# Kernel optimization log

Measured on AMD Instinct MI355X. Metric: run time of the kernel, lower is better.

The kernel has to match this reference:

```python
import jax, jax.numpy as jnp
import numpy as np

N, E, F_IN, H, G, C = 200000, 1000000, 64, 64, 512, 10
EPS = 1e-5


def setup_inputs() -> dict:
    key = jax.random.key(0)
    ks = jax.random.split(key, 16)
    x = jax.random.normal(ks[0], (N, F_IN), dtype=jnp.float32)
    edge_index = jax.random.randint(ks[1], (2, E), 0, N, dtype=jnp.int32)
    batch = jnp.sort(jax.random.randint(ks[2], (N,), 0, G, dtype=jnp.int32))
    def glorot(k, shape):
        lim = np.sqrt(6.0 / (shape[0] + shape[1]))
        return jax.random.uniform(k, shape, jnp.float32, -lim, lim)
    return {
        "x": x, "edge_index": edge_index, "batch": batch,
        "W1": glorot(ks[3], (F_IN, H)), "b1": jnp.zeros((H,), jnp.float32),
        "g1": jnp.ones((H,), jnp.float32), "be1": jnp.zeros((H,), jnp.float32),
        "W2": glorot(ks[4], (H, H)), "b2": jnp.zeros((H,), jnp.float32),
        "g2": jnp.ones((H,), jnp.float32), "be2": jnp.zeros((H,), jnp.float32),
        "lw1": glorot(ks[5], (H, H // 2)), "lb1": jnp.zeros((H // 2,), jnp.float32),
        "lw2": glorot(ks[6], (H // 2, C)), "lb2": jnp.zeros((C,), jnp.float32),
    }


def _gcn_conv(h, src, dst, norm, W, b):
    # PyG GCNConv: linear transform, then normalized gather-scatter aggregation
    h = h @ W                                   # [N, H]
    msg = h[src] * norm[:, None]                # [E+N, H] gather + scale
    out = jax.ops.segment_sum(msg, dst, num_segments=N)  # scatter-add
    return out + b


def _bn_relu(h, g, be):
    m = h.mean(axis=0)
    v = jnp.var(h, axis=0)                      # biased var, as torch BN training
    return jax.nn.relu((h - m) * jax.lax.rsqrt(v + EPS) * g + be)


def reference(x, edge_index, batch, W1, b1, g1, be1, W2, b2, g2, be2,
              lw1, lb1, lw2, lb2):
    loop = jnp.arange(N, dtype=edge_index.dtype)
    src = jnp.concatenate([edge_index[0], loop])  # add self-loops
    dst = jnp.concatenate([edge_index[1], loop])
    deg = jax.ops.segment_sum(jnp.ones_like(src, jnp.float32), dst, num_segments=N)
    dinv = jax.lax.rsqrt(jnp.maximum(deg, 1.0))
    norm = dinv[src] * dinv[dst]                  # sym normalization

    h = _bn_relu(_gcn_conv(x, src, dst, norm, W1, b1), g1, be1)
    prev = h
    h = _bn_relu(_gcn_conv(h, src, dst, norm, W2, b2), g2, be2)
    h = h + prev                                  # residual (dims match)

    # global mean pool over graphs
    sums = jax.ops.segment_sum(h, batch, num_segments=G)        # [G, H]
    cnt = jax.ops.segment_sum(jnp.ones((N,), jnp.float32), batch, num_segments=G)
    pooled = sums / jnp.maximum(cnt, 1.0)[:, None]

    z = jax.nn.relu(pooled @ lw1 + lb1)
    logits = z @ lw2 + lb2                        # [G, C]
    return jax.nn.log_softmax(logits, axis=-1)
```

## Files before the change

kernel.cpp:

```cpp
#include <hip/hip_runtime.h>
#include <hip/hip_bf16.h>
#include <cstdint>
#include <cstddef>

typedef unsigned short u16;
typedef unsigned int u32;
typedef __attribute__((ext_vector_type(8))) short bf16x8;
typedef __attribute__((ext_vector_type(4))) float f32x4;

__device__ __forceinline__ float bf2f(u16 u) {
    return __uint_as_float(((u32)u) << 16);
}
__device__ __forceinline__ float bflo(u32 u) { return __uint_as_float(u << 16); }
__device__ __forceinline__ float bfhi(u32 u) { return __uint_as_float(u & 0xFFFF0000u); }
__device__ __forceinline__ u32 f2bf(float f) {
    u32 b = __float_as_uint(f);
    return (b + 0x7FFFu + ((b >> 16) & 1u)) >> 16;
}

#define CAP 32


__global__ __launch_bounds__(256) void k_fused1(
        const float* __restrict__ X, const float* __restrict__ W,
        const int* __restrict__ ei, int E,
        int* __restrict__ cnt, int* __restrict__ bucket,
        u16* __restrict__ Yb, int nrows, int gemmBlocks) {
    if ((int)blockIdx.x >= gemmBlocks) {
        int e = (blockIdx.x - gemmBlocks) * 256 + threadIdx.x;
        if (e < E) {
            int s = ei[e], d = ei[E + e];
            int pos = atomicAdd(&cnt[d], 1);
            if (pos < CAP) bucket[(size_t)d * CAP + pos] = s;
        }
        return;
    }
    int lane = threadIdx.x & 63;
    int wave = threadIdx.x >> 6;
    int row0 = blockIdx.x * 64 + wave * 16;
    if (row0 >= nrows) return;
    int lrow = lane & 15;
    int lgrp = lane >> 4;

    bf16x8 bfrag[4][2];
#pragma unroll
    for (int c = 0; c < 4; ++c)
#pragma unroll
        for (int h = 0; h < 2; ++h) {
            bf16x8 t;
#pragma unroll
            for (int j = 0; j < 8; ++j)
                t[j] = (short)f2bf(W[(h * 32 + lgrp * 8 + j) * 64 + c * 16 + lrow]);
            bfrag[c][h] = t;
        }

    int arow = min(row0 + lrow, nrows - 1);
    const float* xr = X + (size_t)arow * 64 + lgrp * 8;
    bf16x8 afrag[2];
#pragma unroll
    for (int h = 0; h < 2; ++h) {
        bf16x8 t;
#pragma unroll
        for (int j = 0; j < 8; ++j) t[j] = (short)f2bf(xr[h * 32 + j]);
        afrag[h] = t;
    }

    f32x4 acc[4] = {};
#pragma unroll
    for (int h = 0; h < 2; ++h)
#pragma unroll
        for (int c = 0; c < 4; ++c)
            acc[c] = __builtin_amdgcn_mfma_f32_16x16x32_bf16(afrag[h], bfrag[c][h], acc[c], 0, 0, 0);

#pragma unroll
    for (int j = 0; j < 4; ++j) {
        int r = row0 + lgrp * 4 + j;
        if (r < nrows)
#pragma unroll
            for (int c = 0; c < 4; ++c)
                Yb[(size_t)r * 64 + c * 16 + lrow] = (u16)f2bf(acc[c][j]);
    }
}


__global__ void k_scalelb(u16* __restrict__ HAb, const int* __restrict__ cnt,
                          const int* __restrict__ batch, int* __restrict__ lbound,
                          int N, int G) {
    int idx = blockIdx.x * blockDim.x + threadIdx.x;
    int stride = gridDim.x * blockDim.x;
    int n16 = N * 16;
    uint2* p = (uint2*)HAb;
    for (int i = idx; i < n16; i += stride) {
        int r = i >> 4;
        float dv = rsqrtf((float)(cnt[r] + 1));
        uint2 v = p[i];
        uint2 o;
        o.x = f2bf(bflo(v.x) * dv) | (f2bf(bfhi(v.x) * dv) << 16);
        o.y = f2bf(bflo(v.y) * dv) | (f2bf(bfhi(v.y) * dv) << 16);
        p[i] = o;
    }
    for (int i = idx; i < N; i += stride) {
        int b  = batch[i];
        int bp = (i > 0) ? batch[i - 1] : -1;
        for (int g = bp + 1; g <= b; ++g) lbound[g] = i;
        if (i == N - 1) for (int g = b + 1; g <= G; ++g) lbound[g] = N;
    }
}


__global__ __launch_bounds__(256) void k_gemm2(
        const u16* __restrict__ Xb, const float* __restrict__ W,
        const float* __restrict__ st, const float* __restrict__ g,
        const float* __restrict__ be, const int* __restrict__ cnt,
        u16* __restrict__ Yb, int nrows) {
    __shared__ float ssc[128];
    if (threadIdx.x < 64) {
        int f = threadIdx.x;
        float invn = 1.f / (float)nrows;
        float m   = st[f] * invn;
        float var = st[64 + f] * invn - m * m;
        float scale = g[f] * rsqrtf(var + 1e-5f);
        ssc[f]      = scale;
        ssc[64 + f] = be[f] - m * scale;
    }
    __syncthreads();

    int lane = threadIdx.x & 63;
    int wave = threadIdx.x >> 6;
    int row0 = blockIdx.x * 64 + wave * 16;
    if (row0 >= nrows) return;
    int lrow = lane & 15;
    int lgrp = lane >> 4;

    bf16x8 bfrag[4][2];
#pragma unroll
    for (int c = 0; c < 4; ++c)
#pragma unroll
        for (int h = 0; h < 2; ++h) {
            bf16x8 t;
#pragma unroll
            for (int j = 0; j < 8; ++j)
                t[j] = (short)f2bf(W[(h * 32 + lgrp * 8 + j) * 64 + c * 16 + lrow]);
            bfrag[c][h] = t;
        }

    int arow = min(row0 + lrow, nrows - 1);
    const u16* xr = Xb + (size_t)arow * 64 + lgrp * 8;
    bf16x8 afrag[2];
#pragma unroll
    for (int h = 0; h < 2; ++h) {
        bf16x8 t;
#pragma unroll
        for (int j = 0; j < 8; ++j) {
            int k = h * 32 + lgrp * 8 + j;
            float v = bf2f(xr[h * 32 + j]);
            v = fmaxf(fmaf(v, ssc[k], ssc[64 + k]), 0.f);
            t[j] = (short)f2bf(v);
        }
        afrag[h] = t;
    }

    f32x4 acc[4] = {};
#pragma unroll
    for (int h = 0; h < 2; ++h)
#pragma unroll
        for (int c = 0; c < 4; ++c)
            acc[c] = __builtin_amdgcn_mfma_f32_16x16x32_bf16(afrag[h], bfrag[c][h], acc[c], 0, 0, 0);

#pragma unroll
    for (int j = 0; j < 4; ++j) {
        int r = row0 + lgrp * 4 + j;
        if (r < nrows) {
            float dv = rsqrtf((float)(cnt[r] + 1));
#pragma unroll
            for (int c = 0; c < 4; ++c)
                Yb[(size_t)r * 64 + c * 16 + lrow] = (u16)f2bf(acc[c][j] * dv);
        }
    }
}


__global__ __launch_bounds__(256) void k_gather(
        const u16* __restrict__ HA, const int* __restrict__ cnt,
        const int* __restrict__ bucket, u16* __restrict__ outb,
        float* __restrict__ st, int N) {
    int lane = threadIdx.x & 63;
    int wid  = (blockIdx.x * blockDim.x + threadIdx.x) >> 6;
    int nw   = (gridDim.x * blockDim.x) >> 6;
    float s_ = 0.f, sq_ = 0.f;
    int nb4 = (N + 3) >> 2;
    for (int bt = wid; bt < nb4; bt += nw) {
        int r0 = __builtin_amdgcn_readfirstlane(bt << 2);
        int r1 = min(r0 + 1, N - 1);
        int r2 = min(r0 + 2, N - 1);
        int r3 = min(r0 + 3, N - 1);
        int c0 = cnt[r0], c1 = cnt[r1], c2 = cnt[r2], c3 = cnt[r3];
        int n0 = min(c0, CAP), n1 = min(c1, CAP), n2 = min(c2, CAP), n3 = min(c3, CAP);
        float a0 = bf2f(HA[(size_t)r0 * 64 + lane]);
        float a1 = bf2f(HA[(size_t)r1 * 64 + lane]);
        float a2 = bf2f(HA[(size_t)r2 * 64 + lane]);
        float a3 = bf2f(HA[(size_t)r3 * 64 + lane]);
        const int* bp0 = bucket + (size_t)r0 * CAP;
        const int* bp1 = bucket + (size_t)r1 * CAP;
        const int* bp2 = bucket + (size_t)r2 * CAP;
        const int* bp3 = bucket + (size_t)r3 * CAP;
        int nmax = max(max(n0, n1), max(n2, n3));
        for (int c = 0; c < nmax; c += 8) {
#define IDS(I) \
            int e##I##0 = (c + 0 < n##I) ? bp##I[c + 0] : 0; \
            int e##I##1 = (c + 1 < n##I) ? bp##I[c + 1] : 0; \
            int e##I##2 = (c + 2 < n##I) ? bp##I[c + 2] : 0; \
            int e##I##3 = (c + 3 < n##I) ? bp##I[c + 3] : 0; \
            int e##I##4 = (c + 4 < n##I) ? bp##I[c + 4] : 0; \
            int e##I##5 = (c + 5 < n##I) ? bp##I[c + 5] : 0; \
            int e##I##6 = (c + 6 < n##I) ? bp##I[c + 6] : 0; \
            int e##I##7 = (c + 7 < n##I) ? bp##I[c + 7] : 0;
            IDS(0) IDS(1) IDS(2) IDS(3)
#undef IDS
#define LD(I) \
            float v##I##0 = bf2f(HA[(size_t)e##I##0 * 64 + lane]); \
            float v##I##1 = bf2f(HA[(size_t)e##I##1 * 64 + lane]); \
            float v##I##2 = bf2f(HA[(size_t)e##I##2 * 64 + lane]); \
            float v##I##3 = bf2f(HA[(size_t)e##I##3 * 64 + lane]); \
            float v##I##4 = bf2f(HA[(size_t)e##I##4 * 64 + lane]); \
            float v##I##5 = bf2f(HA[(size_t)e##I##5 * 64 + lane]); \
            float v##I##6 = bf2f(HA[(size_t)e##I##6 * 64 + lane]); \
            float v##I##7 = bf2f(HA[(size_t)e##I##7 * 64 + lane]);
            LD(0) LD(1) LD(2) LD(3)
#undef LD
#define ACCUM(I) \
            a##I += (c + 0 < n##I) ? v##I##0 : 0.f; \
            a##I += (c + 1 < n##I) ? v##I##1 : 0.f; \
            a##I += (c + 2 < n##I) ? v##I##2 : 0.f; \
            a##I += (c + 3 < n##I) ? v##I##3 : 0.f; \
            a##I += (c + 4 < n##I) ? v##I##4 : 0.f; \
            a##I += (c + 5 < n##I) ? v##I##5 : 0.f; \
            a##I += (c + 6 < n##I) ? v##I##6 : 0.f; \
            a##I += (c + 7 < n##I) ? v##I##7 : 0.f;
            ACCUM(0) ACCUM(1) ACCUM(2) ACCUM(3)
#undef ACCUM
        }
        float d0 = rsqrtf((float)(c0 + 1));
        float d1 = rsqrtf((float)(c1 + 1));
        float d2 = rsqrtf((float)(c2 + 1));
        float d3 = rsqrtf((float)(c3 + 1));
        {
            u16 u = (u16)f2bf(a0 * d0);
            outb[(size_t)r0 * 64 + lane] = u;
            float vr = bf2f(u); s_ += vr; sq_ += vr * vr;
        }
        if (r0 + 1 < N) {
            u16 u = (u16)f2bf(a1 * d1);
            outb[(size_t)r1 * 64 + lane] = u;
            float vr = bf2f(u); s_ += vr; sq_ += vr * vr;
        }
        if (r0 + 2 < N) {
            u16 u = (u16)f2bf(a2 * d2);
            outb[(size_t)r2 * 64 + lane] = u;
            float vr = bf2f(u); s_ += vr; sq_ += vr * vr;
        }
        if (r0 + 3 < N) {
            u16 u = (u16)f2bf(a3 * d3);
            outb[(size_t)r3 * 64 + lane] = u;
            float vr = bf2f(u); s_ += vr; sq_ += vr * vr;
        }
    }
    __shared__ float ls[4][64], lq[4][64];
    int grp = threadIdx.x >> 6;
    ls[grp][lane] = s_; lq[grp][lane] = sq_;
    __syncthreads();
    if (grp == 0) {
        s_  = ls[0][lane] + ls[1][lane] + ls[2][lane] + ls[3][lane];
        sq_ = lq[0][lane] + lq[1][lane] + lq[2][lane] + lq[3][lane];
        unsafeAtomicAdd(&st[lane], s_);
        unsafeAtomicAdd(&st[64 + lane], sq_);
    }
}


__global__ void k_pool(const u16* __restrict__ rb2, const float* __restrict__ st2,
                       const float* __restrict__ g2, const float* __restrict__ be2,
                       const u16* __restrict__ rb1, const float* __restrict__ st1,
                       const float* __restrict__ g1, const float* __restrict__ be1,
                       const int* __restrict__ batch, float* __restrict__ psum, int N) {
    __shared__ float s1[128], s2[128];
    if (threadIdx.x < 64) {
        int f = threadIdx.x;
        float invn = 1.f / (float)N;
        float m   = st2[f] * invn;
        float var = st2[64 + f] * invn - m * m;
        float scale = g2[f] * rsqrtf(var + 1e-5f);
        s2[f] = scale; s2[64 + f] = be2[f] - m * scale;
    } else if (threadIdx.x < 128) {
        int f = threadIdx.x - 64;
        float invn = 1.f / (float)N;
        float m   = st1[f] * invn;
        float var = st1[64 + f] * invn - m * m;
        float scale = g1[f] * rsqrtf(var + 1e-5f);
        s1[f] = scale; s1[64 + f] = be1[f] - m * scale;
    }
    __syncthreads();

    int lane = threadIdx.x & 63;
    int wv   = (blockIdx.x * blockDim.x + threadIdx.x) >> 6;
    int r0   = wv * 64;
    if (r0 >= N) return;
    int rend = min(r0 + 64, N);
    int bv = (r0 + lane < N) ? batch[r0 + lane] : -1;
    float s2a = s2[lane], s2b = s2[64 + lane];
    float s1a = s1[lane], s1b = s1[64 + lane];
    float acc = 0.f;
    int cur = __shfl(bv, 0, 64);
    for (int r = r0; r < rend; ++r) {
        int b = __shfl(bv, r - r0, 64);
        if (b != cur) {
            unsafeAtomicAdd(&psum[(size_t)cur * 64 + lane], acc);
            acc = 0.f; cur = b;
        }
        float v2 = fmaxf(fmaf(bf2f(rb2[(size_t)r * 64 + lane]), s2a, s2b), 0.f);
        float v1 = fmaxf(fmaf(bf2f(rb1[(size_t)r * 64 + lane]), s1a, s1b), 0.f);
        acc += v1 + v2;
    }
    unsafeAtomicAdd(&psum[(size_t)cur * 64 + lane], acc);
}


__global__ void k_head(const float* __restrict__ psum, const int* __restrict__ lbound,
                       const float* __restrict__ lw1, const float* __restrict__ lb1,
                       const float* __restrict__ lw2, const float* __restrict__ lb2,
                       float* __restrict__ out, int G) {
    int g = blockIdx.x * blockDim.x + threadIdx.x;
    if (g >= G) return;
    float cnt = (float)(lbound[g + 1] - lbound[g]);
    float inv = 1.f / fmaxf(cnt, 1.f);
    float p[64];
#pragma unroll
    for (int f = 0; f < 64; ++f) p[f] = psum[(size_t)g * 64 + f] * inv;
    float z[32];
#pragma unroll
    for (int j = 0; j < 32; ++j) {
        float a = lb1[j];
#pragma unroll
        for (int f = 0; f < 64; ++f) a = fmaf(p[f], lw1[f * 32 + j], a);
        z[j] = fmaxf(a, 0.f);
    }
    float lg[10];
    float mx = -1e30f;
#pragma unroll
    for (int c = 0; c < 10; ++c) {
        float a = lb2[c];
#pragma unroll
        for (int j = 0; j < 32; ++j) a = fmaf(z[j], lw2[j * 10 + c], a);
        lg[c] = a;
        mx = fmaxf(mx, a);
    }
    float se = 0.f;
#pragma unroll
    for (int c = 0; c < 10; ++c) se += expf(lg[c] - mx);
    float lse = logf(se) + mx;
#pragma unroll
    for (int c = 0; c < 10; ++c) out[(size_t)g * 10 + c] = lg[c] - lse;
}


extern "C" void kernel_launch(void* const* d_in, const int* in_sizes, int n_in,
                              void* d_out, int out_size, void* d_ws, size_t ws_size,
                              hipStream_t stream) {
    const float* x    = (const float*)d_in[0];
    const int*   ei   = (const int*)d_in[1];
    const int*   batch= (const int*)d_in[2];
    const float* W1   = (const float*)d_in[3];
    const float* g1   = (const float*)d_in[5];
    const float* be1  = (const float*)d_in[6];
    const float* W2   = (const float*)d_in[7];
    const float* g2   = (const float*)d_in[9];
    const float* be2  = (const float*)d_in[10];
    const float* lw1  = (const float*)d_in[11];
    const float* lb1  = (const float*)d_in[12];
    const float* lw2  = (const float*)d_in[13];
    const float* lb2  = (const float*)d_in[14];
    float* out = (float*)d_out;

    const int N = in_sizes[2];
    const int E = in_sizes[1] / 2;
    const int C = 10;
    const int G = out_size / C;

    char* wp = (char*)d_ws;
    auto carve = [&wp](size_t bytes) -> char* {
        uintptr_t u = ((uintptr_t)wp + 63) & ~(uintptr_t)63;
        char* r = (char*)u;
        wp = r + bytes;
        return r;
    };
    int*   cnt   = (int*)carve((size_t)N * 4);
    float* st1   = (float*)carve(128 * 4);
    float* st2   = (float*)carve(128 * 4);
    float* psum  = (float*)carve((size_t)G * 64 * 4);
    size_t zone  = (char*)(psum + (size_t)G * 64) - (char*)cnt;
    int*   lbound= (int*)carve((size_t)(G + 1) * 4);
    int*   bucket= (int*)carve((size_t)N * CAP * 4);
    u16*   HAbf  = (u16*)carve((size_t)N * 64 * 2);
    u16*   Rb1   = (u16*)carve((size_t)N * 64 * 2);
    u16*   Rb2   = (u16*)carve((size_t)N * 64 * 2);

    hipMemsetAsync(cnt, 0, zone, stream);

    const int gemmBlocks = (N + 63) / 64;
    const int fillBlocks = (E + 255) / 256;

    k_fused1<<<gemmBlocks + fillBlocks, 256, 0, stream>>>(
        x, W1, ei, E, cnt, bucket, HAbf, N, gemmBlocks);

    k_scalelb<<<2048, 256, 0, stream>>>(HAbf, cnt, batch, lbound, N, G);

    k_gather<<<4096, 256, 0, stream>>>(HAbf, cnt, bucket, Rb1, st1, N);

    k_gemm2<<<gemmBlocks, 256, 0, stream>>>(Rb1, W2, st1, g1, be1, cnt, HAbf, N);

    k_gather<<<4096, 256, 0, stream>>>(HAbf, cnt, bucket, Rb2, st2, N);

    {
        int waves = (N + 63) / 64;
        int blocks = (waves + 3) / 4;
        k_pool<<<blocks, 256, 0, stream>>>(Rb2, st2, g2, be2, Rb1, st1, g1, be1,
                                           batch, psum, N);
    }

    k_head<<<(G + 255) / 256, 256, 0, stream>>>(psum, lbound, lw1, lb1, lw2, lb2, out, G);
}
```

Baseline: 415.6 us.

## Transpose edge buckets to slot-major and fold degree scaling into first GEMM

Stores neighbor buckets slot-major so the gather loads four rows' neighbor ids with one vector read per slot. Splits the bucket fill from the first GEMM so the GEMM can apply the inverse-sqrt-degree scaling in its epilogue, removing the separate rescale pass over the feature matrix. Graph boundaries for mean pooling are now found by binary search in the head kernel instead of a precomputed array. Bucket fill writes become strided across nodes, and the extra kernel boundary serializes the fill and GEMM.

```diff
diff --git a/kernel.cpp b/kernel.cpp
--- a/kernel.cpp
+++ b/kernel.cpp
@@ -21,20 +21,19 @@
 #define CAP 32
 
 
-__global__ __launch_bounds__(256) void k_fused1(
+__global__ void k_bfill(const int* __restrict__ ei, int E, int N,
+                        int* __restrict__ cnt, int* __restrict__ bucket) {
+    int e = blockIdx.x * blockDim.x + threadIdx.x;
+    if (e >= E) return;
+    int s = ei[e], d = ei[E + e];
+    int pos = atomicAdd(&cnt[d], 1);
+    if (pos < CAP) bucket[(size_t)pos * N + d] = s;
+}
+
+
+__global__ __launch_bounds__(256) void k_gemm1(
         const float* __restrict__ X, const float* __restrict__ W,
-        const int* __restrict__ ei, int E,
-        int* __restrict__ cnt, int* __restrict__ bucket,
-        u16* __restrict__ Yb, int nrows, int gemmBlocks) {
-    if ((int)blockIdx.x >= gemmBlocks) {
-        int e = (blockIdx.x - gemmBlocks) * 256 + threadIdx.x;
-        if (e < E) {
-            int s = ei[e], d = ei[E + e];
-            int pos = atomicAdd(&cnt[d], 1);
-            if (pos < CAP) bucket[(size_t)d * CAP + pos] = s;
-        }
-        return;
-    }
+        const int* __restrict__ cnt, u16* __restrict__ Yb, int nrows) {
     int lane = threadIdx.x & 63;
     int wave = threadIdx.x >> 6;
     int row0 = blockIdx.x * 64 + wave * 16;
@@ -75,35 +74,12 @@
 #pragma unroll
     for (int j = 0; j < 4; ++j) {
         int r = row0 + lgrp * 4 + j;
-        if (r < nrows)
+        if (r < nrows) {
+            float dv = rsqrtf((float)(cnt[r] + 1));
 #pragma unroll
             for (int c = 0; c < 4; ++c)
-                Yb[(size_t)r * 64 + c * 16 + lrow] = (u16)f2bf(acc[c][j]);
-    }
-}
-
-
-__global__ void k_scalelb(u16* __restrict__ HAb, const int* __restrict__ cnt,
-                          const int* __restrict__ batch, int* __restrict__ lbound,
-                          int N, int G) {
-    int idx = blockIdx.x * blockDim.x + threadIdx.x;
-    int stride = gridDim.x * blockDim.x;
-    int n16 = N * 16;
-    uint2* p = (uint2*)HAb;
-    for (int i = idx; i < n16; i += stride) {
-        int r = i >> 4;
-        float dv = rsqrtf((float)(cnt[r] + 1));
-        uint2 v = p[i];
-        uint2 o;
-        o.x = f2bf(bflo(v.x) * dv) | (f2bf(bfhi(v.x) * dv) << 16);
-        o.y = f2bf(bflo(v.y) * dv) | (f2bf(bfhi(v.y) * dv) << 16);
-        p[i] = o;
-    }
-    for (int i = idx; i < N; i += stride) {
-        int b  = batch[i];
-        int bp = (i > 0) ? batch[i - 1] : -1;
-        for (int g = bp + 1; g <= b; ++g) lbound[g] = i;
-        if (i == N - 1) for (int g = b + 1; g <= G; ++g) lbound[g] = N;
+                Yb[(size_t)r * 64 + c * 16 + lrow] = (u16)f2bf(acc[c][j] * dv);
+        }
     }
 }
 
@@ -189,6 +165,7 @@
     int nw   = (gridDim.x * blockDim.x) >> 6;
     float s_ = 0.f, sq_ = 0.f;
     int nb4 = (N + 3) >> 2;
+    u32 nm1 = (u32)(N - 1);
     for (int bt = wid; bt < nb4; bt += nw) {
         int r0 = __builtin_amdgcn_readfirstlane(bt << 2);
         int r1 = min(r0 + 1, N - 1);
@@ -200,44 +177,33 @@
         float a1 = bf2f(HA[(size_t)r1 * 64 + lane]);
         float a2 = bf2f(HA[(size_t)r2 * 64 + lane]);
         float a3 = bf2f(HA[(size_t)r3 * 64 + lane]);
-        const int* bp0 = bucket + (size_t)r0 * CAP;
-        const int* bp1 = bucket + (size_t)r1 * CAP;
-        const int* bp2 = bucket + (size_t)r2 * CAP;
-        const int* bp3 = bucket + (size_t)r3 * CAP;
         int nmax = max(max(n0, n1), max(n2, n3));
         for (int c = 0; c < nmax; c += 8) {
-#define IDS(I) \
-            int e##I##0 = (c + 0 < n##I) ? bp##I[c + 0] : 0; \
-            int e##I##1 = (c + 1 < n##I) ? bp##I[c + 1] : 0; \
-            int e##I##2 = (c + 2 < n##I) ? bp##I[c + 2] : 0; \
-            int e##I##3 = (c + 3 < n##I) ? bp##I[c + 3] : 0; \
-            int e##I##4 = (c + 4 < n##I) ? bp##I[c + 4] : 0; \
-            int e##I##5 = (c + 5 < n##I) ? bp##I[c + 5] : 0; \
-            int e##I##6 = (c + 6 < n##I) ? bp##I[c + 6] : 0; \
-            int e##I##7 = (c + 7 < n##I) ? bp##I[c + 7] : 0;
-            IDS(0) IDS(1) IDS(2) IDS(3)
-#undef IDS
-#define LD(I) \
-            float v##I##0 = bf2f(HA[(size_t)e##I##0 * 64 + lane]); \
-            float v##I##1 = bf2f(HA[(size_t)e##I##1 * 64 + lane]); \
-            float v##I##2 = bf2f(HA[(size_t)e##I##2 * 64 + lane]); \
-            float v##I##3 = bf2f(HA[(size_t)e##I##3 * 64 + lane]); \
-            float v##I##4 = bf2f(HA[(size_t)e##I##4 * 64 + lane]); \
-            float v##I##5 = bf2f(HA[(size_t)e##I##5 * 64 + lane]); \
-            float v##I##6 = bf2f(HA[(size_t)e##I##6 * 64 + lane]); \
-            float v##I##7 = bf2f(HA[(size_t)e##I##7 * 64 + lane]);
-            LD(0) LD(1) LD(2) LD(3)
-#undef LD
-#define ACCUM(I) \
-            a##I += (c + 0 < n##I) ? v##I##0 : 0.f; \
-            a##I += (c + 1 < n##I) ? v##I##1 : 0.f; \
-            a##I += (c + 2 < n##I) ? v##I##2 : 0.f; \
-            a##I += (c + 3 < n##I) ? v##I##3 : 0.f; \
-            a##I += (c + 4 < n##I) ? v##I##4 : 0.f; \
-            a##I += (c + 5 < n##I) ? v##I##5 : 0.f; \
-            a##I += (c + 6 < n##I) ? v##I##6 : 0.f; \
-            a##I += (c + 7 < n##I) ? v##I##7 : 0.f;
-            ACCUM(0) ACCUM(1) ACCUM(2) ACCUM(3)
+#define SLOT(K) int4 q##K = *(const int4*)(bucket + (size_t)(c + K) * N + r0);
+            SLOT(0) SLOT(1) SLOT(2) SLOT(3) SLOT(4) SLOT(5) SLOT(6) SLOT(7)
+#undef SLOT
+#define EDGE(K, I) \
+            u32 id##K##I = (c + K < n##I) ? (u32)((&q##K.x)[I]) : 0u; \
+            id##K##I = min(id##K##I, nm1); \
+            float v##K##I = bf2f(HA[(size_t)id##K##I * 64 + lane]);
+            EDGE(0,0) EDGE(0,1) EDGE(0,2) EDGE(0,3)
+            EDGE(1,0) EDGE(1,1) EDGE(1,2) EDGE(1,3)
+            EDGE(2,0) EDGE(2,1) EDGE(2,2) EDGE(2,3)
+            EDGE(3,0) EDGE(3,1) EDGE(3,2) EDGE(3,3)
+            EDGE(4,0) EDGE(4,1) EDGE(4,2) EDGE(4,3)
+            EDGE(5,0) EDGE(5,1) EDGE(5,2) EDGE(5,3)
+            EDGE(6,0) EDGE(6,1) EDGE(6,2) EDGE(6,3)
+            EDGE(7,0) EDGE(7,1) EDGE(7,2) EDGE(7,3)
+#undef EDGE
+#define ACCUM(K, I) a##I += (c + K < n##I) ? v##K##I : 0.f;
+            ACCUM(0,0) ACCUM(1,0) ACCUM(2,0) ACCUM(3,0)
+            ACCUM(4,0) ACCUM(5,0) ACCUM(6,0) ACCUM(7,0)
+            ACCUM(0,1) ACCUM(1,1) ACCUM(2,1) ACCUM(3,1)
+            ACCUM(4,1) ACCUM(5,1) ACCUM(6,1) ACCUM(7,1)
+            ACCUM(0,2) ACCUM(1,2) ACCUM(2,2) ACCUM(3,2)
+            ACCUM(4,2) ACCUM(5,2) ACCUM(6,2) ACCUM(7,2)
+            ACCUM(0,3) ACCUM(1,3) ACCUM(2,3) ACCUM(3,3)
+            ACCUM(4,3) ACCUM(5,3) ACCUM(6,3) ACCUM(7,3)
 #undef ACCUM
         }
         float d0 = rsqrtf((float)(c0 + 1));
@@ -325,13 +291,18 @@
 }
 
 
-__global__ void k_head(const float* __restrict__ psum, const int* __restrict__ lbound,
+__global__ void k_head(const float* __restrict__ psum, const int* __restrict__ batch,
                        const float* __restrict__ lw1, const float* __restrict__ lb1,
                        const float* __restrict__ lw2, const float* __restrict__ lb2,
-                       float* __restrict__ out, int G) {
+                       float* __restrict__ out, int N, int G) {
     int g = blockIdx.x * blockDim.x + threadIdx.x;
     if (g >= G) return;
-    float cnt = (float)(lbound[g + 1] - lbound[g]);
+    int lo = 0, hi = N;
+    while (lo < hi) { int mid = (lo + hi) >> 1; if (batch[mid] < g) lo = mid + 1; else hi = mid; }
+    int lb = lo;
+    hi = N;
+    while (lo < hi) { int mid = (lo + hi) >> 1; if (batch[mid] < g + 1) lo = mid + 1; else hi = mid; }
+    float cnt = (float)(lo - lb);
     float inv = 1.f / fmaxf(cnt, 1.f);
     float p[64];
 #pragma unroll
@@ -398,8 +369,7 @@
     float* st2   = (float*)carve(128 * 4);
     float* psum  = (float*)carve((size_t)G * 64 * 4);
     size_t zone  = (char*)(psum + (size_t)G * 64) - (char*)cnt;
-    int*   lbound= (int*)carve((size_t)(G + 1) * 4);
-    int*   bucket= (int*)carve((size_t)N * CAP * 4);
+    int*   bucket= (int*)carve(((size_t)N * CAP + 16) * 4);
     u16*   HAbf  = (u16*)carve((size_t)N * 64 * 2);
     u16*   Rb1   = (u16*)carve((size_t)N * 64 * 2);
     u16*   Rb2   = (u16*)carve((size_t)N * 64 * 2);
@@ -407,17 +377,13 @@
     hipMemsetAsync(cnt, 0, zone, stream);
 
     const int gemmBlocks = (N + 63) / 64;
-    const int fillBlocks = (E + 255) / 256;
-
-    k_fused1<<<gemmBlocks + fillBlocks, 256, 0, stream>>>(
-        x, W1, ei, E, cnt, bucket, HAbf, N, gemmBlocks);
-
-    k_scalelb<<<2048, 256, 0, stream>>>(HAbf, cnt, batch, lbound, N, G);
-
+
+    k_bfill<<<(E + 255) / 256, 256, 0, stream>>>(ei, E, N, cnt, bucket);
+
+    k_gemm1<<<gemmBlocks, 256, 0, stream>>>(x, W1, cnt, HAbf, N);
     k_gather<<<4096, 256, 0, stream>>>(HAbf, cnt, bucket, Rb1, st1, N);
 
     k_gemm2<<<gemmBlocks, 256, 0, stream>>>(Rb1, W2, st1, g1, be1, cnt, HAbf, N);
-
     k_gather<<<4096, 256, 0, stream>>>(HAbf, cnt, bucket, Rb2, st2, N);
 
     {
@@ -427,5 +393,6 @@
                                            batch, psum, N);
     }
 
-    k_head<<<(G + 255) / 256, 256, 0, stream>>>(psum, lbound, lw1, lb1, lw2, lb2, out, G);
-}
+    k_head<<<(G + 255) / 256, 256, 0, stream>>>(psum, batch, lw1, lb1, lw2, lb2,
+                                                out, N, G);
+}
```

Measured after the change: 401.1 us, median of 2. 1.04x faster.
